# Kernel optimization log

Hardware: AMD Instinct MI355X
Metric: run time of the kernel (lower is better)

The kernel has to match this reference:

```python
import jax, jax.numpy as jnp
import numpy as np

D_MODEL = 512
D_STATE = 64
D_CONV = 4
EXPAND = 2
D_INNER = EXPAND * D_MODEL  # 1024
DT_RANK = D_MODEL // 16     # 32 (mamba default: ceil(d_model/16))
BATCH = 1
SEQ = 2048


def setup_inputs() -> dict:
    key = jax.random.key(0)
    ks = jax.random.split(key, 10)
    def n(k, shape, scale):
        return jax.random.normal(k, shape, dtype=jnp.float32) * scale
    x = n(ks[0], (BATCH, SEQ, D_MODEL), 1.0)
    ln_g = jnp.ones((D_MODEL,), jnp.float32)
    ln_b = jnp.zeros((D_MODEL,), jnp.float32)
    Win = n(ks[1], (2 * D_INNER, D_MODEL), D_MODEL ** -0.5)
    conv_w = n(ks[2], (D_INNER, 1, D_CONV), 0.5)      # depthwise kernel (O,I/g,K)
    conv_b = n(ks[3], (D_INNER,), 0.02)
    Wx = n(ks[4], (DT_RANK + 2 * D_STATE, D_INNER), D_INNER ** -0.5)
    Wdt = n(ks[5], (D_INNER, DT_RANK), DT_RANK ** -0.5)
    bdt = n(ks[6], (D_INNER,), 0.02)
    # Mamba S4D-real init: A = 1..d_state repeated per channel
    A_log = jnp.log(jnp.tile(jnp.arange(1, D_STATE + 1, dtype=jnp.float32)[None, :], (D_INNER, 1)))
    Dp = jnp.ones((D_INNER,), jnp.float32)
    Wout = n(ks[7], (D_MODEL, D_INNER), D_INNER ** -0.5)
    return dict(x=x, ln_g=ln_g, ln_b=ln_b, Win=Win, conv_w=conv_w, conv_b=conv_b,
                Wx=Wx, Wdt=Wdt, bdt=bdt, A_log=A_log, Dp=Dp, Wout=Wout)


def _layernorm(x, g, b, eps=1e-5):
    mu = jnp.mean(x, axis=-1, keepdims=True)
    xc = x - mu
    var = jnp.mean(xc * xc, axis=-1, keepdims=True)
    return xc * jax.lax.rsqrt(var + eps) * g + b


def _mamba_block(x, ln_g, ln_b, Win, conv_w, conv_b, Wx, Wdt, bdt, A_log, Dp, Wout):
    residual = x
    xn = _layernorm(x, ln_g, ln_b)
    # in_proj -> (x, z) gates
    xz = jnp.einsum('bld,ed->ble', xn, Win)           # (B,L,2*D_INNER)
    xi, z = jnp.split(xz, 2, axis=-1)
    # causal depthwise conv1d (torch pads d_conv-1 both sides then truncates to L == left-pad only)
    xc = jnp.transpose(xi, (0, 2, 1))                 # (B,C,L)
    xc = jax.lax.conv_general_dilated(
        xc, conv_w, window_strides=(1,), padding=[(D_CONV - 1, 0)],
        dimension_numbers=('NCH', 'OIH', 'NCH'), feature_group_count=D_INNER)
    xc = xc + conv_b[None, :, None]
    xi = jax.nn.silu(jnp.transpose(xc, (0, 2, 1)))    # (B,L,D_INNER)
    # x_proj -> dt, B, C
    dbc = jnp.einsum('bld,ed->ble', xi, Wx)           # (B,L,DT_RANK+2N)
    dt = dbc[..., :DT_RANK]
    Bm = dbc[..., DT_RANK:DT_RANK + D_STATE]          # (B,L,N)
    Cm = dbc[..., DT_RANK + D_STATE:]                 # (B,L,N)
    delta = jax.nn.softplus(jnp.einsum('blr,dr->bld', dt, Wdt) + bdt)  # (B,L,D_INNER)
    A = -jnp.exp(A_log)                               # (D_INNER,N), negative
    dA = jnp.exp(delta[..., None] * A)                # (B,L,D_INNER,N) in (0,1)
    dBx = (delta * xi)[..., None] * Bm[:, :, None, :] # (B,L,D_INNER,N)
    def step(h, t):
        dA_t, dBx_t, C_t = t
        h = dA_t * h + dBx_t                          # (B,D_INNER,N)
        y_t = jnp.einsum('bdn,bn->bd', h, C_t)
        return h, y_t
    h0 = jnp.zeros((x.shape[0], D_INNER, D_STATE), x.dtype)
    _, ys = jax.lax.scan(step, h0, (jnp.transpose(dA, (1, 0, 2, 3)),
                                    jnp.transpose(dBx, (1, 0, 2, 3)),
                                    jnp.transpose(Cm, (1, 0, 2))))
    y = jnp.transpose(ys, (1, 0, 2)) + Dp * xi        # skip term D*x
    y = y * jax.nn.silu(z)                            # gate
    out = jnp.einsum('bld,ed->ble', y, Wout)          # out_proj
    return out + residual


def reference(x, ln_g, ln_b, Win, conv_w, conv_b, Wx, Wdt, bdt, A_log, Dp, Wout):
    return _mamba_block(x, ln_g, ln_b, Win, conv_w, conv_b, Wx, Wdt, bdt, A_log, Dp, Wout)
```

## Files before the change

kernel.cpp:

```cpp
#include <hip/hip_runtime.h>
#include <hip/hip_bf16.h>
#include <cstddef>

#define SEQ 2048
#define DM  512
#define DI  1024
#define DR  32
#define DS  64
#define NCHUNK 32
#define CHUNK  64
#define MB (1024 * 1024)
#define NCVT 1696

typedef __attribute__((ext_vector_type(4))) float f32x4;
typedef __attribute__((ext_vector_type(8))) short frag8;

__device__ __forceinline__ unsigned short f2bf(float f) {
    unsigned u = __float_as_uint(f);
    unsigned r = (u + 0x7fffu + ((u >> 16) & 1u)) >> 16;
    return (unsigned short)r;
}
__device__ __forceinline__ float bf2f(unsigned short u) {
    return __int_as_float(((int)u) << 16);
}

__device__ __forceinline__ float fexp2(float x) {
#if __has_builtin(__builtin_amdgcn_exp2f)
    return __builtin_amdgcn_exp2f(x);
#else
    return exp2f(x);
#endif
}
#define LOG2E 1.44269504088896f

template <int CTRL>
__device__ __forceinline__ float dppadd(float p) {
    return p + __int_as_float(
        __builtin_amdgcn_update_dpp(0, __float_as_int(p), CTRL, 0xF, 0xF, true));
}

__global__ void cvt_ln(const float* __restrict__ w1, unsigned short* __restrict__ o1,
                       const float* __restrict__ w2, unsigned short* __restrict__ o2,
                       const float* __restrict__ w3, unsigned short* __restrict__ o3,
                       const float* __restrict__ x, const float* __restrict__ g,
                       const float* __restrict__ b, unsigned short* __restrict__ xn) {
    if (blockIdx.x < NCVT) {
        const int n1 = 1048576, n2 = 163840, n3 = 524288;
        int i = (blockIdx.x * 256 + threadIdx.x) * 4;
        const float* s; unsigned short* d; int off;
        if (i < n1) { s = w1; d = o1; off = i; }
        else if (i < n1 + n2) { s = w2; d = o2; off = i - n1; }
        else if (i < n1 + n2 + n3) { s = w3; d = o3; off = i - n1 - n2; }
        else return;
        float4 v = *(const float4*)(s + off);
        ushort4 o = { f2bf(v.x), f2bf(v.y), f2bf(v.z), f2bf(v.w) };
        *(ushort4*)(d + off) = o;
        return;
    }
    int l = blockIdx.x - NCVT;
    int t = threadIdx.x;
    __shared__ float red[256];
    float v0 = x[l * DM + t];
    float v1 = x[l * DM + t + 256];
    red[t] = v0 + v1;
    __syncthreads();
    for (int o = 128; o > 0; o >>= 1) { if (t < o) red[t] += red[t + o]; __syncthreads(); }
    float mu = red[0] * (1.f / DM);
    __syncthreads();
    float c0 = v0 - mu, c1 = v1 - mu;
    red[t] = c0 * c0 + c1 * c1;
    __syncthreads();
    for (int o = 128; o > 0; o >>= 1) { if (t < o) red[t] += red[t + o]; __syncthreads(); }
    float rstd = rsqrtf(red[0] * (1.f / DM) + 1e-5f);
    xn[l * DM + t]       = f2bf(c0 * rstd * g[t]       + b[t]);
    xn[l * DM + t + 256] = f2bf(c1 * rstd * g[t + 256] + b[t + 256]);
}

#define LDK 40

template <int EPI>
__global__ __launch_bounds__(256, 2)
void gemm_bf(const unsigned short* __restrict__ A, int lda,
             const unsigned short* __restrict__ B, int ldb,
             int N, int K,
             float* __restrict__ outF, const float* __restrict__ res, int ldo,
             float* __restrict__ dtc, unsigned short* __restrict__ bci,
             unsigned short* __restrict__ outB1, unsigned short* __restrict__ outB2) {
    __shared__ unsigned short As[128 * LDK];
    __shared__ unsigned short Bs[64 * LDK];
    int t = threadIdx.x;
    int lane = t & 63;
    int wv = t >> 6;
    int wm = (wv >> 1) * 64;
    int wn = (wv & 1) * 32;
    int m0 = blockIdx.x * 128, n0 = blockIdx.y * 64;

    f32x4 acc[4][2];
#pragma unroll
    for (int i = 0; i < 4; i++)
#pragma unroll
        for (int j = 0; j < 2; j++) acc[i][j] = (f32x4){0.f, 0.f, 0.f, 0.f};

    int lm = lane & 15;
    int kq = (lane >> 4) * 8;

    for (int k0 = 0; k0 < K; k0 += 32) {
#pragma unroll
        for (int j = 0; j < 2; j++) {
            int c = t + j * 256;
            int m = c >> 2;
            int k = (c & 3) * 8;
            frag8 v = *(const frag8*)(A + (size_t)(m0 + m) * lda + k0 + k);
            *(frag8*)(&As[m * LDK + k]) = v;
        }
        {
            int m = t >> 2;
            int k = (t & 3) * 8;
            int gn = n0 + m;
            frag8 v = {0, 0, 0, 0, 0, 0, 0, 0};
            if (gn < N) v = *(const frag8*)(B + (size_t)gn * ldb + k0 + k);
            *(frag8*)(&Bs[m * LDK + k]) = v;
        }
        __syncthreads();

        frag8 af[4], bfr[2];
#pragma unroll
        for (int mt = 0; mt < 4; mt++)
            af[mt] = *(const frag8*)(&As[(wm + mt * 16 + lm) * LDK + kq]);
#pragma unroll
        for (int nt = 0; nt < 2; nt++)
            bfr[nt] = *(const frag8*)(&Bs[(wn + nt * 16 + lm) * LDK + kq]);
#pragma unroll
        for (int mt = 0; mt < 4; mt++)
#pragma unroll
            for (int nt = 0; nt < 2; nt++)
                acc[mt][nt] = __builtin_amdgcn_mfma_f32_16x16x32_bf16(
                    af[mt], bfr[nt], acc[mt][nt], 0, 0, 0);
        __syncthreads();
    }

    int rbase = (lane >> 4) * 4;
#pragma unroll
    for (int mt = 0; mt < 4; mt++) {
#pragma unroll
        for (int nt = 0; nt < 2; nt++) {
            int n = n0 + wn + nt * 16 + lm;
            int mb = m0 + wm + mt * 16 + rbase;
            if (EPI == 1) {
                if (n < DI) {
#pragma unroll
                    for (int r = 0; r < 4; r++)
                        outB1[(size_t)(mb + r) * DI + n] = f2bf(acc[mt][nt][r]);
                } else {
                    int nn = n - DI;
                    ushort4 o;
#pragma unroll
                    for (int r = 0; r < 4; r++) {
                        float v = acc[mt][nt][r];
                        v = v / (1.f + __expf(-v));
                        (&o.x)[r] = f2bf(v);
                    }
                    *(ushort4*)(outB2 + (size_t)nn * SEQ + mb) = o;
                }
            } else if (EPI == 2) {
                if (n < N) {
#pragma unroll
                    for (int r = 0; r < 4; r++)
                        outF[(size_t)(mb + r) * ldo + n] =
                            acc[mt][nt][r] + res[(size_t)(mb + r) * ldo + n];
                }
            } else {
                if (n < 32) {
#pragma unroll
                    for (int r = 0; r < 4; r++)
                        dtc[(size_t)(mb + r) * 32 + n] = acc[mt][nt][r];
                } else if (n < 96) {
                    int col = 2 * (n - 32);
#pragma unroll
                    for (int r = 0; r < 4; r++)
                        bci[(size_t)(mb + r) * 128 + col] = f2bf(acc[mt][nt][r]);
                } else if (n < 160) {
                    int col = 2 * (n - 96) + 1;
#pragma unroll
                    for (int r = 0; r < 4; r++)
                        bci[(size_t)(mb + r) * 128 + col] = f2bf(acc[mt][nt][r]);
                }
            }
        }
    }
}

__global__ void gemm_dt_t(const float* __restrict__ A,
                          const float* __restrict__ B,
                          const float* __restrict__ bias,
                          float* __restrict__ outT) {
    __shared__ float As[16][65];
    __shared__ float Bs[16][65];
    int tid = threadIdx.x;
    int tx = tid & 15, ty = tid >> 4;
    int bm = blockIdx.x * 64, bn = blockIdx.y * 64;
    float acc[4][4] = {};
    int kk = tid & 15;
    int rr = tid >> 4;
    for (int k0 = 0; k0 < DR; k0 += 16) {
#pragma unroll
        for (int i = 0; i < 4; i++)
            As[kk][rr + 16 * i] = A[(size_t)(bm + rr + 16 * i) * 32 + k0 + kk];
#pragma unroll
        for (int i = 0; i < 4; i++)
            Bs[kk][rr + 16 * i] = B[(size_t)(bn + rr + 16 * i) * DR + k0 + kk];
        __syncthreads();
#pragma unroll
        for (int k = 0; k < 16; k++) {
            float a[4], bb[4];
#pragma unroll
            for (int i = 0; i < 4; i++) a[i] = As[k][ty * 4 + i];
#pragma unroll
            for (int j = 0; j < 4; j++) bb[j] = Bs[k][tx * 4 + j];
#pragma unroll
            for (int i = 0; i < 4; i++)
#pragma unroll
                for (int j = 0; j < 4; j++)
                    acc[i][j] = fmaf(a[i], bb[j], acc[i][j]);
        }
        __syncthreads();
    }
#pragma unroll
    for (int j = 0; j < 4; j++) {
        int e = bn + tx * 4 + j;
        float bv = bias[e];
        float4 o;
#pragma unroll
        for (int i = 0; i < 4; i++) {
            float v = acc[i][j] + bv;
            v = (v > 20.f) ? v : __logf(1.f + __expf(v));
            (&o.x)[i] = v;
        }
        *(float4*)(outT + (size_t)e * SEQ + bm + ty * 4) = o;
    }
}

__global__ void conv_t(const unsigned short* __restrict__ xi_raw,
                       const float* __restrict__ w, const float* __restrict__ cb,
                       unsigned short* __restrict__ xi2bf, unsigned short* __restrict__ xi2T) {
    __shared__ float tin[67][72];
    __shared__ float tout[64][65];
    int l0 = blockIdx.x * 64, e0 = blockIdx.y * 64;
    int t = threadIdx.x;
    for (int c = t; c < 536; c += 256) {
        int r = c >> 3, ke = (c & 7) * 8;
        int l = l0 - 3 + r;
        frag8 v = {0, 0, 0, 0, 0, 0, 0, 0};
        if (l >= 0) v = *(const frag8*)(xi_raw + (size_t)l * DI + e0 + ke);
#pragma unroll
        for (int i = 0; i < 8; i++) tin[r][ke + i] = bf2f((unsigned short)v[i]);
    }
    __syncthreads();
    int e_loc = t & 63;
    int e = e0 + e_loc;
    float4 wv = *(const float4*)(w + e * 4);
    float bias = cb[e];
#pragma unroll 4
    for (int i = 0; i < 16; i++) {
        int l_loc = (t >> 6) + i * 4;
        float acc = bias;
        acc = fmaf(wv.x, tin[l_loc][e_loc], acc);
        acc = fmaf(wv.y, tin[l_loc + 1][e_loc], acc);
        acc = fmaf(wv.z, tin[l_loc + 2][e_loc], acc);
        acc = fmaf(wv.w, tin[l_loc + 3][e_loc], acc);
        float s = acc / (1.f + __expf(-acc));
        tout[l_loc][e_loc] = s;
        xi2bf[(size_t)(l0 + l_loc) * DI + e] = f2bf(s);
    }
    __syncthreads();
    for (int c = t; c < 1024; c += 256) {
        int er = c >> 4, l4 = (c & 15) * 4;
        ushort4 o = { f2bf(tout[l4][er]), f2bf(tout[l4 + 1][er]),
                      f2bf(tout[l4 + 2][er]), f2bf(tout[l4 + 3][er]) };
        *(ushort4*)(xi2T + (size_t)(e0 + er) * SEQ + l0 + l4) = o;
    }
}

__global__ void scan_passA(const float* __restrict__ deltaT, const unsigned short* __restrict__ xi2T,
                           const unsigned short* __restrict__ bci, const float* __restrict__ A_log,
                           float* __restrict__ sumd, float* __restrict__ hend) {
    int wid = blockIdx.x * 4 + (threadIdx.x >> 6);
    int eg = wid & 255;
    int c  = wid >> 8;
    int lane = threadIdx.x & 63;
    int g = lane >> 4;
    int i = lane & 15;
    int e = eg * 4 + g;
    int l0 = c * CHUNK;
    float4 al = *(const float4*)(A_log + e * DS + 4 * i);
    float Ae2[4];
#pragma unroll
    for (int k = 0; k < 4; k++) Ae2[k] = -__expf((&al.x)[k]) * LOG2E;
    float h[4] = {0.f, 0.f, 0.f, 0.f};
    float sum_d = 0.f;
    const float4* d4  = (const float4*)(deltaT + (size_t)e * SEQ + l0);
    const ushort4* x4 = (const ushort4*)(xi2T + (size_t)e * SEQ + l0);
    const uint4* bc4  = (const uint4*)((const unsigned*)bci + (size_t)l0 * 64) + i;
    for (int gq = 0; gq < CHUNK / 4; gq++) {
        float4 dd = d4[gq];
        ushort4 xx = x4[gq];
#pragma unroll
        for (int j = 0; j < 4; j++) {
            uint4 bcv = bc4[(4 * gq + j) * 16];
            float dj = (&dd.x)[j];
            float dx = dj * bf2f((&xx.x)[j]);
            sum_d += dj;
#pragma unroll
            for (int k = 0; k < 4; k++) {
                float dA = fexp2(dj * Ae2[k]);
                float Bk = __int_as_float((&bcv.x)[k] << 16);
                h[k] = fmaf(dA, h[k], dx * Bk);
            }
        }
    }
    size_t idx = ((size_t)c * DI + e) * DS + 4 * i;
    float4 hv = {h[0], h[1], h[2], h[3]};
    *(float4*)(hend + idx) = hv;
    if (i == 0) sumd[c * DI + e] = sum_d;
}

__global__ void scan_carry(float* __restrict__ hend, const float* __restrict__ sumd,
                           const float* __restrict__ A_log) {
    int e = blockIdx.x * 4 + (threadIdx.x >> 6);
    int n = threadIdx.x & 63;
    float Ae2 = -__expf(A_log[e * DS + n]) * LOG2E;
    float he[NCHUNK - 1], sd[NCHUNK - 1];
#pragma unroll
    for (int c = 0; c < NCHUNK - 1; c++)
        he[c] = hend[((size_t)c * DI + e) * DS + n];
#pragma unroll
    for (int c = 0; c < NCHUNK - 1; c++)
        sd[c] = sumd[c * DI + e];
    float h = 0.f;
#pragma unroll
    for (int c = 0; c < NCHUNK - 1; c++) {
        float P = fexp2(Ae2 * sd[c]);
        hend[((size_t)c * DI + e) * DS + n] = h;
        h = fmaf(P, h, he[c]);
    }
    hend[((size_t)(NCHUNK - 1) * DI + e) * DS + n] = h;
}

__global__ void scan_passB(const float* __restrict__ deltaT, const unsigned short* __restrict__ xi2T,
                           const unsigned short* __restrict__ bci, const unsigned short* __restrict__ szT,
                           const float* __restrict__ A_log, const float* __restrict__ Dp,
                           const float* __restrict__ hin, unsigned short* __restrict__ y_bf) {
    int wid = blockIdx.x * 4 + (threadIdx.x >> 6);
    int eg = wid & 255;
    int c  = wid >> 8;
    int lane = threadIdx.x & 63;
    int g = lane >> 4;
    int i = lane & 15;
    int e = eg * 4 + g;
    int l0 = c * CHUNK;
    float4 al = *(const float4*)(A_log + e * DS + 4 * i);
    float Ae2[4];
#pragma unroll
    for (int k = 0; k < 4; k++) Ae2[k] = -__expf((&al.x)[k]) * LOG2E;
    float dp = Dp[e];
    float4 hv = *(const float4*)(hin + ((size_t)c * DI + e) * DS + 4 * i);
    float h[4] = {hv.x, hv.y, hv.z, hv.w};
    const float4* d4  = (const float4*)(deltaT + (size_t)e * SEQ + l0);
    const ushort4* x4 = (const ushort4*)(xi2T + (size_t)e * SEQ + l0);
    const ushort4* s4 = (const ushort4*)(szT + (size_t)e * SEQ + l0);
    const uint4* bc4  = (const uint4*)((const unsigned*)bci + (size_t)l0 * 64) + i;
    for (int gq = 0; gq < CHUNK / 4; gq++) {
        float4 dd = d4[gq];
        ushort4 xx = x4[gq], zz = s4[gq];
        ushort4 yv;
#pragma unroll
        for (int j = 0; j < 4; j++) {
            uint4 bcv = bc4[(4 * gq + j) * 16];
            float dj = (&dd.x)[j];
            float xj = bf2f((&xx.x)[j]);
            float dx = dj * xj;
            float Ck[4];
#pragma unroll
            for (int k = 0; k < 4; k++) {
                unsigned w = (&bcv.x)[k];
                float Bk = __int_as_float(w << 16);
                Ck[k] = __int_as_float(w & 0xffff0000u);
                float dA = fexp2(dj * Ae2[k]);
                h[k] = fmaf(dA, h[k], dx * Bk);
            }
            float p = h[0] * Ck[0];
            p = fmaf(h[1], Ck[1], p);
            p = fmaf(h[2], Ck[2], p);
            p = fmaf(h[3], Ck[3], p);
            p = dppadd<0xB1>(p);
            p = dppadd<0x4E>(p);
            p = dppadd<0x141>(p);
            p = dppadd<0x140>(p);
            (&yv.x)[j] = f2bf((p + dp * xj) * bf2f((&zz.x)[j]));
        }
        if (i == 0) {
#pragma unroll
            for (int j = 0; j < 4; j++)
                y_bf[(size_t)(l0 + 4 * gq + j) * DI + e] = (&yv.x)[j];
        }
    }
}

extern "C" void kernel_launch(void* const* d_in, const int* in_sizes, int n_in,
                              void* d_out, int out_size, void* d_ws, size_t ws_size,
                              hipStream_t stream) {
    const float* x      = (const float*)d_in[0];
    const float* ln_g   = (const float*)d_in[1];
    const float* ln_b   = (const float*)d_in[2];
    const float* Win    = (const float*)d_in[3];
    const float* conv_w = (const float*)d_in[4];
    const float* conv_b = (const float*)d_in[5];
    const float* Wx     = (const float*)d_in[6];
    const float* Wdt    = (const float*)d_in[7];
    const float* bdt    = (const float*)d_in[8];
    const float* A_log  = (const float*)d_in[9];
    const float* Dp     = (const float*)d_in[10];
    const float* Wout   = (const float*)d_in[11];
    float* out = (float*)d_out;

    char* W = (char*)d_ws;
    unsigned short* xi_raw  = (unsigned short*)W;
    float*          deltaT  = (float*)W;
    unsigned short* Win_bf  = (unsigned short*)(W + 8 * MB);
    unsigned short* xi2bf   = (unsigned short*)(W + 8 * MB);
    unsigned short* y_bf    = (unsigned short*)(W + 8 * MB);
    unsigned short* szT     = (unsigned short*)(W + 12 * MB);
    unsigned short* xi2T    = (unsigned short*)(W + 16 * MB);
    unsigned short* xn_bf   = (unsigned short*)(W + 20 * MB);
    float*          hend    = (float*)(W + 20 * MB);
    unsigned short* Wout_bf = (unsigned short*)(W + 28 * MB);
    float*          sumd    = (float*)(W + 29 * MB);
    unsigned short* Wx_bf   = (unsigned short*)(W + 29 * MB + 128 * 1024);
    float*          dtc     = (float*)(W + 29 * MB + 448 * 1024);
    unsigned short* bci     = (unsigned short*)(W + 29 * MB + 704 * 1024);

    cvt_ln<<<NCVT + SEQ, 256, 0, stream>>>(Win, Win_bf, Wx, Wx_bf, Wout, Wout_bf,
                                           x, ln_g, ln_b, xn_bf);

    gemm_bf<1><<<dim3(SEQ / 128, 2048 / 64), 256, 0, stream>>>(
        xn_bf, DM, Win_bf, DM, 2048, DM, nullptr, nullptr, 0, nullptr, nullptr,
        xi_raw, szT);

    conv_t<<<dim3(SEQ / 64, DI / 64), 256, 0, stream>>>(xi_raw, conv_w, conv_b, xi2bf, xi2T);

    gemm_bf<4><<<dim3(SEQ / 128, 3), 256, 0, stream>>>(
        xi2bf, DI, Wx_bf, DI, 160, DI, nullptr, nullptr, 0, dtc, bci, nullptr, nullptr);

    gemm_dt_t<<<dim3(SEQ / 64, DI / 64), 256, 0, stream>>>(dtc, Wdt, bdt, deltaT);

    scan_passA<<<(DI / 4) * (NCHUNK - 1) / 4, 256, 0, stream>>>(deltaT, xi2T, bci, A_log, sumd, hend);
    scan_carry<<<DI / 4, 256, 0, stream>>>(hend, sumd, A_log);
    scan_passB<<<(DI / 4) * NCHUNK / 4, 256, 0, stream>>>(deltaT, xi2T, bci, szT,
                                                          A_log, Dp, hend, y_bf);

    gemm_bf<2><<<dim3(SEQ / 128, DM / 64), 256, 0, stream>>>(
        y_bf, DI, Wout_bf, DI, DM, DI, out, x, DM, nullptr, nullptr, nullptr, nullptr);
}
```

Measured before the change: 236.2 us.

## Store scan B/C in fp32 separate arrays and vectorize scan with packed float2 math

The x_proj epilogue now writes B and C as separate fp32 arrays instead of an interleaved bf16 array. The scan kernels read them as float4, preload four timesteps of B/C per group, and use float2 vector ops, which the compiler may lower to packed FMA. In pass B the DPP cross-lane reductions are batched across the four timesteps, and both scan kernels gain launch bounds for occupancy. This removes bf16 unpacking and serialized reductions, but doubles the B/C memory traffic.

```diff
diff --git a/kernel.cpp b/kernel.cpp
--- a/kernel.cpp
+++ b/kernel.cpp
@@ -13,6 +13,7 @@
 #define NCVT 1696
 
 typedef __attribute__((ext_vector_type(4))) float f32x4;
+typedef __attribute__((ext_vector_type(2))) float f32x2;
 typedef __attribute__((ext_vector_type(8))) short frag8;
 
 __device__ __forceinline__ unsigned short f2bf(float f) {
@@ -34,9 +35,13 @@
 #define LOG2E 1.44269504088896f
 
 template <int CTRL>
-__device__ __forceinline__ float dppadd(float p) {
-    return p + __int_as_float(
-        __builtin_amdgcn_update_dpp(0, __float_as_int(p), CTRL, 0xF, 0xF, true));
+__device__ __forceinline__ f32x2 dppadd2(f32x2 p) {
+    f32x2 t;
+    t.x = __int_as_float(
+        __builtin_amdgcn_update_dpp(0, __float_as_int(p.x), CTRL, 0xF, 0xF, true));
+    t.y = __int_as_float(
+        __builtin_amdgcn_update_dpp(0, __float_as_int(p.y), CTRL, 0xF, 0xF, true));
+    return p + t;
 }
 
 __global__ void cvt_ln(const float* __restrict__ w1, unsigned short* __restrict__ o1,
@@ -84,7 +89,7 @@
              const unsigned short* __restrict__ B, int ldb,
              int N, int K,
              float* __restrict__ outF, const float* __restrict__ res, int ldo,
-             float* __restrict__ dtc, unsigned short* __restrict__ bci,
+             float* __restrict__ dtc, float* __restrict__ Bfp, float* __restrict__ Cfp,
              unsigned short* __restrict__ outB1, unsigned short* __restrict__ outB2) {
     __shared__ unsigned short As[128 * LDK];
     __shared__ unsigned short Bs[64 * LDK];
@@ -175,15 +180,13 @@
                     for (int r = 0; r < 4; r++)
                         dtc[(size_t)(mb + r) * 32 + n] = acc[mt][nt][r];
                 } else if (n < 96) {
-                    int col = 2 * (n - 32);
 #pragma unroll
                     for (int r = 0; r < 4; r++)
-                        bci[(size_t)(mb + r) * 128 + col] = f2bf(acc[mt][nt][r]);
+                        Bfp[(size_t)(mb + r) * DS + (n - 32)] = acc[mt][nt][r];
                 } else if (n < 160) {
-                    int col = 2 * (n - 96) + 1;
 #pragma unroll
                     for (int r = 0; r < 4; r++)
-                        bci[(size_t)(mb + r) * 128 + col] = f2bf(acc[mt][nt][r]);
+                        Cfp[(size_t)(mb + r) * DS + (n - 96)] = acc[mt][nt][r];
                 }
             }
         }
@@ -281,9 +284,10 @@
     }
 }
 
-__global__ void scan_passA(const float* __restrict__ deltaT, const unsigned short* __restrict__ xi2T,
-                           const unsigned short* __restrict__ bci, const float* __restrict__ A_log,
-                           float* __restrict__ sumd, float* __restrict__ hend) {
+__global__ __launch_bounds__(256, 4)
+void scan_passA(const float* __restrict__ deltaT, const unsigned short* __restrict__ xi2T,
+                const float* __restrict__ Bf, const float* __restrict__ A_log,
+                float* __restrict__ sumd, float* __restrict__ hend) {
     int wid = blockIdx.x * 4 + (threadIdx.x >> 6);
     int eg = wid & 255;
     int c  = wid >> 8;
@@ -293,33 +297,37 @@
     int e = eg * 4 + g;
     int l0 = c * CHUNK;
     float4 al = *(const float4*)(A_log + e * DS + 4 * i);
-    float Ae2[4];
-#pragma unroll
-    for (int k = 0; k < 4; k++) Ae2[k] = -__expf((&al.x)[k]) * LOG2E;
-    float h[4] = {0.f, 0.f, 0.f, 0.f};
+    f32x2 nA01 = { -__expf(al.x) * LOG2E, -__expf(al.y) * LOG2E };
+    f32x2 nA23 = { -__expf(al.z) * LOG2E, -__expf(al.w) * LOG2E };
+    f32x2 h01 = {0.f, 0.f}, h23 = {0.f, 0.f};
     float sum_d = 0.f;
     const float4* d4  = (const float4*)(deltaT + (size_t)e * SEQ + l0);
     const ushort4* x4 = (const ushort4*)(xi2T + (size_t)e * SEQ + l0);
-    const uint4* bc4  = (const uint4*)((const unsigned*)bci + (size_t)l0 * 64) + i;
+    const float4* b4  = (const float4*)(Bf + (size_t)l0 * DS) + i;
     for (int gq = 0; gq < CHUNK / 4; gq++) {
         float4 dd = d4[gq];
         ushort4 xx = x4[gq];
+        float4 Bv[4];
+#pragma unroll
+        for (int j = 0; j < 4; j++) Bv[j] = b4[(4 * gq + j) * 16];
 #pragma unroll
         for (int j = 0; j < 4; j++) {
-            uint4 bcv = bc4[(4 * gq + j) * 16];
             float dj = (&dd.x)[j];
+            f32x2 dj2 = {dj, dj};
+            f32x2 e01 = dj2 * nA01, e23 = dj2 * nA23;
+            f32x2 dA01, dA23;
+            dA01.x = fexp2(e01.x); dA01.y = fexp2(e01.y);
+            dA23.x = fexp2(e23.x); dA23.y = fexp2(e23.y);
             float dx = dj * bf2f((&xx.x)[j]);
+            f32x2 dx2 = {dx, dx};
             sum_d += dj;
-#pragma unroll
-            for (int k = 0; k < 4; k++) {
-                float dA = fexp2(dj * Ae2[k]);
-                float Bk = __int_as_float((&bcv.x)[k] << 16);
-                h[k] = fmaf(dA, h[k], dx * Bk);
-            }
+            f32x2 B01 = {Bv[j].x, Bv[j].y}, B23 = {Bv[j].z, Bv[j].w};
+            h01 = dA01 * h01 + dx2 * B01;
+            h23 = dA23 * h23 + dx2 * B23;
         }
     }
     size_t idx = ((size_t)c * DI + e) * DS + 4 * i;
-    float4 hv = {h[0], h[1], h[2], h[3]};
+    float4 hv = {h01.x, h01.y, h23.x, h23.y};
     *(float4*)(hend + idx) = hv;
     if (i == 0) sumd[c * DI + e] = sum_d;
 }
@@ -346,10 +354,12 @@
     hend[((size_t)(NCHUNK - 1) * DI + e) * DS + n] = h;
 }
 
-__global__ void scan_passB(const float* __restrict__ deltaT, const unsigned short* __restrict__ xi2T,
-                           const unsigned short* __restrict__ bci, const unsigned short* __restrict__ szT,
-                           const float* __restrict__ A_log, const float* __restrict__ Dp,
-                           const float* __restrict__ hin, unsigned short* __restrict__ y_bf) {
+__global__ __launch_bounds__(256, 4)
+void scan_passB(const float* __restrict__ deltaT, const unsigned short* __restrict__ xi2T,
+                const float* __restrict__ Bf, const float* __restrict__ Cf,
+                const unsigned short* __restrict__ szT,
+                const float* __restrict__ A_log, const float* __restrict__ Dp,
+                const float* __restrict__ hin, unsigned short* __restrict__ y_bf) {
     int wid = blockIdx.x * 4 + (threadIdx.x >> 6);
     int eg = wid & 255;
     int c  = wid >> 8;
@@ -359,49 +369,62 @@
     int e = eg * 4 + g;
     int l0 = c * CHUNK;
     float4 al = *(const float4*)(A_log + e * DS + 4 * i);
-    float Ae2[4];
-#pragma unroll
-    for (int k = 0; k < 4; k++) Ae2[k] = -__expf((&al.x)[k]) * LOG2E;
+    f32x2 nA01 = { -__expf(al.x) * LOG2E, -__expf(al.y) * LOG2E };
+    f32x2 nA23 = { -__expf(al.z) * LOG2E, -__expf(al.w) * LOG2E };
     float dp = Dp[e];
     float4 hv = *(const float4*)(hin + ((size_t)c * DI + e) * DS + 4 * i);
-    float h[4] = {hv.x, hv.y, hv.z, hv.w};
+    f32x2 h01 = {hv.x, hv.y}, h23 = {hv.z, hv.w};
     const float4* d4  = (const float4*)(deltaT + (size_t)e * SEQ + l0);
     const ushort4* x4 = (const ushort4*)(xi2T + (size_t)e * SEQ + l0);
     const ushort4* s4 = (const ushort4*)(szT + (size_t)e * SEQ + l0);
-    const uint4* bc4  = (const uint4*)((const unsigned*)bci + (size_t)l0 * 64) + i;
+    const float4* b4  = (const float4*)(Bf + (size_t)l0 * DS) + i;
+    const float4* c4  = (const float4*)(Cf + (size_t)l0 * DS) + i;
     for (int gq = 0; gq < CHUNK / 4; gq++) {
         float4 dd = d4[gq];
         ushort4 xx = x4[gq], zz = s4[gq];
-        ushort4 yv;
+        float4 Bv[4], Cv[4];
 #pragma unroll
         for (int j = 0; j < 4; j++) {
-            uint4 bcv = bc4[(4 * gq + j) * 16];
+            Bv[j] = b4[(4 * gq + j) * 16];
+            Cv[j] = c4[(4 * gq + j) * 16];
+        }
+        float ps[4], xs[4];
+#pragma unroll
+        for (int j = 0; j < 4; j++) {
             float dj = (&dd.x)[j];
+            f32x2 dj2 = {dj, dj};
+            f32x2 e01 = dj2 * nA01, e23 = dj2 * nA23;
+            f32x2 dA01, dA23;
+            dA01.x = fexp2(e01.x); dA01.y = fexp2(e01.y);
+            dA23.x = fexp2(e23.x); dA23.y = fexp2(e23.y);
             float xj = bf2f((&xx.x)[j]);
             float dx = dj * xj;
-            float Ck[4];
-#pragma unroll
-            for (int k = 0; k < 4; k++) {
-                unsigned w = (&bcv.x)[k];
-                float Bk = __int_as_float(w << 16);
-                Ck[k] = __int_as_float(w & 0xffff0000u);
-                float dA = fexp2(dj * Ae2[k]);
-                h[k] = fmaf(dA, h[k], dx * Bk);
-            }
-            float p = h[0] * Ck[0];
-            p = fmaf(h[1], Ck[1], p);
-            p = fmaf(h[2], Ck[2], p);
-            p = fmaf(h[3], Ck[3], p);
-            p = dppadd<0xB1>(p);
-            p = dppadd<0x4E>(p);
-            p = dppadd<0x141>(p);
-            p = dppadd<0x140>(p);
-            (&yv.x)[j] = f2bf((p + dp * xj) * bf2f((&zz.x)[j]));
-        }
+            f32x2 dx2 = {dx, dx};
+            f32x2 B01 = {Bv[j].x, Bv[j].y}, B23 = {Bv[j].z, Bv[j].w};
+            h01 = dA01 * h01 + dx2 * B01;
+            h23 = dA23 * h23 + dx2 * B23;
+            f32x2 C01 = {Cv[j].x, Cv[j].y}, C23 = {Cv[j].z, Cv[j].w};
+            f32x2 pp = h01 * C01;
+            pp = h23 * C23 + pp;
+            ps[j] = pp.x + pp.y;
+            xs[j] = xj;
+        }
+        f32x2 q01 = {ps[0], ps[1]}, q23 = {ps[2], ps[3]};
+        q01 = dppadd2<0xB1>(q01);  q23 = dppadd2<0xB1>(q23);
+        q01 = dppadd2<0x4E>(q01);  q23 = dppadd2<0x4E>(q23);
+        q01 = dppadd2<0x141>(q01); q23 = dppadd2<0x141>(q23);
+        q01 = dppadd2<0x140>(q01); q23 = dppadd2<0x140>(q23);
+        f32x2 x01 = {xs[0], xs[1]}, x23 = {xs[2], xs[3]};
+        f32x2 z01 = {bf2f(zz.x), bf2f(zz.y)}, z23 = {bf2f(zz.z), bf2f(zz.w)};
+        f32x2 dp2 = {dp, dp};
+        f32x2 y01 = (q01 + dp2 * x01) * z01;
+        f32x2 y23 = (q23 + dp2 * x23) * z23;
         if (i == 0) {
-#pragma unroll
-            for (int j = 0; j < 4; j++)
-                y_bf[(size_t)(l0 + 4 * gq + j) * DI + e] = (&yv.x)[j];
+            size_t base = (size_t)(l0 + 4 * gq) * DI + e;
+            y_bf[base]          = f2bf(y01.x);
+            y_bf[base + DI]     = f2bf(y01.y);
+            y_bf[base + 2 * DI] = f2bf(y23.x);
+            y_bf[base + 3 * DI] = f2bf(y23.y);
         }
     }
 }
@@ -437,27 +460,29 @@
     float*          sumd    = (float*)(W + 29 * MB);
     unsigned short* Wx_bf   = (unsigned short*)(W + 29 * MB + 128 * 1024);
     float*          dtc     = (float*)(W + 29 * MB + 448 * 1024);
-    unsigned short* bci     = (unsigned short*)(W + 29 * MB + 704 * 1024);
+    float*          Bf      = (float*)(W + 29 * MB + 704 * 1024);
+    float*          Cf      = Bf + (size_t)SEQ * DS;
 
     cvt_ln<<<NCVT + SEQ, 256, 0, stream>>>(Win, Win_bf, Wx, Wx_bf, Wout, Wout_bf,
                                            x, ln_g, ln_b, xn_bf);
 
     gemm_bf<1><<<dim3(SEQ / 128, 2048 / 64), 256, 0, stream>>>(
-        xn_bf, DM, Win_bf, DM, 2048, DM, nullptr, nullptr, 0, nullptr, nullptr,
+        xn_bf, DM, Win_bf, DM, 2048, DM, nullptr, nullptr, 0, nullptr, nullptr, nullptr,
         xi_raw, szT);
 
     conv_t<<<dim3(SEQ / 64, DI / 64), 256, 0, stream>>>(xi_raw, conv_w, conv_b, xi2bf, xi2T);
 
     gemm_bf<4><<<dim3(SEQ / 128, 3), 256, 0, stream>>>(
-        xi2bf, DI, Wx_bf, DI, 160, DI, nullptr, nullptr, 0, dtc, bci, nullptr, nullptr);
+        xi2bf, DI, Wx_bf, DI, 160, DI, nullptr, nullptr, 0, dtc, Bf, Cf, nullptr, nullptr);
 
     gemm_dt_t<<<dim3(SEQ / 64, DI / 64), 256, 0, stream>>>(dtc, Wdt, bdt, deltaT);
 
-    scan_passA<<<(DI / 4) * (NCHUNK - 1) / 4, 256, 0, stream>>>(deltaT, xi2T, bci, A_log, sumd, hend);
+    scan_passA<<<(DI / 4) * (NCHUNK - 1) / 4, 256, 0, stream>>>(deltaT, xi2T, Bf, A_log, sumd, hend);
     scan_carry<<<DI / 4, 256, 0, stream>>>(hend, sumd, A_log);
-    scan_passB<<<(DI / 4) * NCHUNK / 4, 256, 0, stream>>>(deltaT, xi2T, bci, szT,
+    scan_passB<<<(DI / 4) * NCHUNK / 4, 256, 0, stream>>>(deltaT, xi2T, Bf, Cf, szT,
                                                           A_log, Dp, hend, y_bf);
 
     gemm_bf<2><<<dim3(SEQ / 128, DM / 64), 256, 0, stream>>>(
-        y_bf, DI, Wout_bf, DI, DM, DI, out, x, DM, nullptr, nullptr, nullptr, nullptr);
-}
+        y_bf, DI, Wout_bf, DI, DM, DI, out, x, DM, nullptr, nullptr, nullptr,
+        nullptr, nullptr);
+}
```

Result: slower. 240.9 us (+2.0%).
